# Optimization experiments

Measured on AMD Instinct MI355X. Metric: run time of the kernel, lower is better.

The kernel has to match this reference:

```python
import jax, jax.numpy as jnp
import numpy as np

N = 2048      # number of ROIs
C = 1024      # in_channels == inter_channels
G = 16        # groups
D = C // G    # per-group dim = 64


def _bbox_overlaps(b1, b2):
    # mmdet-1.x IoU with +1 pixel convention; b1:(N,4), b2:(M,4)
    area1 = (b1[:, 2] - b1[:, 0] + 1) * (b1[:, 3] - b1[:, 1] + 1)  # (N,)
    area2 = (b2[:, 2] - b2[:, 0] + 1) * (b2[:, 3] - b2[:, 1] + 1)  # (M,)
    lt = jnp.maximum(b1[:, None, :2], b2[None, :, :2])             # (N,M,2)
    rb = jnp.minimum(b1[:, None, 2:], b2[None, :, 2:])             # (N,M,2)
    wh = jnp.clip(rb - lt + 1, 0)
    inter = wh[..., 0] * wh[..., 1]                                # (N,M)
    return inter / (area1[:, None] + area2[None, :] - inter)


def setup_inputs() -> dict:
    key = jax.random.key(0)
    ks = jax.random.split(key, 9)
    in_x = jax.random.normal(ks[0], (N, C), dtype=jnp.float32)
    # valid boxes: [batch_idx, x1, y1, x2, y2]
    xy = jax.random.uniform(ks[1], (N, 2), minval=0.0, maxval=800.0)
    wh = jax.random.uniform(ks[2], (N, 2), minval=8.0, maxval=200.0)
    rois = jnp.concatenate([jnp.zeros((N, 1)), xy, xy + wh], axis=1).astype(jnp.float32)
    s = 1.0 / np.sqrt(C)
    W0 = jax.random.normal(ks[3], (C, C), dtype=jnp.float32) * s
    b0 = jnp.zeros((C,), dtype=jnp.float32)
    W1 = jax.random.normal(ks[4], (C, C), dtype=jnp.float32) * s
    b1 = jnp.zeros((C,), dtype=jnp.float32)
    # grouped 1x1 conv: per group maps C channels -> D channels
    Wout = jax.random.normal(ks[5], (G, D, C), dtype=jnp.float32) * s
    bout = jnp.zeros((C,), dtype=jnp.float32)
    return {"in_x": in_x, "rois": rois, "W0": W0, "b0": b0, "W1": W1,
            "b1": b1, "Wout": Wout, "bout": bout}


def reference(in_x, rois, W0, b0, W1, b1, Wout, bout):
    # self-attention path: in_ref_x = in_x, ref_rois = rois
    # embed convs are pre-activation (relu -> 1x1 conv), shared for x and ref_x
    def embed(v):
        v = jax.nn.relu(v) @ W0.T + b0
        v = jax.nn.relu(v) @ W1.T + b1
        return v
    x = embed(in_x)                      # (N, C)
    ref_x = x                            # shared convs, same input
    xg = x.reshape(N, G, D)
    rg = ref_x.reshape(N, G, D)
    scores = jnp.einsum('ngd,mgd->ngm', xg, rg) / jnp.sqrt(jnp.float32(D))  # (N,G,N)
    ious = _bbox_overlaps(rois[:, 1:], rois[:, 1:])                          # (N,N)
    scores = scores + jnp.log(ious[:, None, :] + 1e-6)
    attn = jax.nn.softmax(scores, axis=2)                                    # (N,G,N)
    y = jnp.einsum('ngm,mc->ngc', attn, in_x)                                # (N,G,C)
    out = jnp.einsum('ngc,goc->ngo', y, Wout).reshape(N, C) + bout           # (N,C)
    return out
```

## Files before the change

kernel.cpp:

```cpp
#include <hip/hip_runtime.h>
#include <math.h>

constexpr int NROI = 2048;
constexpr int CDIM = 1024;
constexpr int NG   = 16;
constexpr int DH   = 64;

typedef __attribute__((ext_vector_type(8))) short short8;
typedef __attribute__((ext_vector_type(4))) float floatx4;

#define MFMA_BF16(a, b, c) __builtin_amdgcn_mfma_f32_16x16x32_bf16((a), (b), (c), 0, 0, 0)

__device__ __forceinline__ short f2bf(float f) {
  unsigned u = __float_as_uint(f);
  unsigned r = 0x7fffu + ((u >> 16) & 1u);
  return (short)((u + r) >> 16);
}
__device__ __forceinline__ float bf2f(unsigned short u) {
  return __uint_as_float(((unsigned)u) << 16);
}
__device__ __forceinline__ unsigned pack2(float a, float b) {
  return (unsigned)(unsigned short)f2bf(a) | ((unsigned)(unsigned short)f2bf(b) << 16);
}

__device__ __forceinline__ unsigned cvtpk_bf16(float lo, float hi) {
  unsigned r;
  asm("v_cvt_pk_bf16_f32 %0, %1, %2" : "=v"(r) : "v"(lo), "v"(hi));
  return r;
}

__device__ __forceinline__ float fexp2(float x) {
#if __has_builtin(__builtin_amdgcn_exp2f)
  return __builtin_amdgcn_exp2f(x);
#else
  return __expf(x * 0.69314718056f);
#endif
}

typedef __attribute__((address_space(1))) void GV;
typedef __attribute__((address_space(3))) void LV;
__device__ __forceinline__ void gl2lds16(const void* g, void* l) {
  __builtin_amdgcn_global_load_lds((GV*)g, (LV*)l, 16, 0, 0);
}

__device__ __forceinline__ short8 brelu(short8 v) {
  union { short8 s; unsigned u[4]; } x; x.s = v;
#pragma unroll
  for (int i = 0; i < 4; ++i) {
    unsigned m = (x.u[i] >> 15) & 0x10001u;
    x.u[i] &= ~(m * 0xFFFFu);
  }
  return x.s;
}

__device__ __forceinline__ int keypos(int k) {
  return (k & ~31) | (((k >> 2) & 3) << 3) | (((k >> 4) & 1) << 2);
}

__global__ __launch_bounds__(256) void convert_kernel(
    const float* __restrict__ in_x, const float* __restrict__ W0,
    const float* __restrict__ W1, const float* __restrict__ Wout,
    short* __restrict__ xin_b, short* __restrict__ W0b,
    short* __restrict__ W1b, short* __restrict__ Woutb)
{
  const int i = blockIdx.x * 256 + threadIdx.x;
  {
    const float4 v = ((const float4*)in_x)[i];
    uint2 u; u.x = pack2(v.x, v.y); u.y = pack2(v.z, v.w);
    ((uint2*)xin_b)[i] = u;
  }
  if (i < 262144) {
    float4 v = ((const float4*)W0)[i];
    uint2 u; u.x = pack2(v.x, v.y); u.y = pack2(v.z, v.w);
    ((uint2*)W0b)[i] = u;
    v = ((const float4*)W1)[i];
    u.x = pack2(v.x, v.y); u.y = pack2(v.z, v.w);
    ((uint2*)W1b)[i] = u;
    v = ((const float4*)Wout)[i];
    u.x = pack2(v.x, v.y); u.y = pack2(v.z, v.w);
    ((uint2*)Woutb)[i] = u;
  }
}

__global__ __launch_bounds__(256) void iou4_kernel(const float* __restrict__ rois,
                                                   unsigned short* __restrict__ biasb)
{
  const int q  = blockIdx.y;
  const int k0 = (blockIdx.x * 256 + threadIdx.x) * 4;
  const float qx1 = rois[q * 5 + 1], qy1 = rois[q * 5 + 2];
  const float qx2 = rois[q * 5 + 3], qy2 = rois[q * 5 + 4];
  const float qa = (qx2 - qx1 + 1.f) * (qy2 - qy1 + 1.f);
  float v[4];
#pragma unroll
  for (int j = 0; j < 4; ++j) {
    const int k = k0 + j;
    const float kx1 = rois[k * 5 + 1], ky1 = rois[k * 5 + 2];
    const float kx2 = rois[k * 5 + 3], ky2 = rois[k * 5 + 4];
    const float ka = (kx2 - kx1 + 1.f) * (ky2 - ky1 + 1.f);
    float iw = fminf(qx2, kx2) - fmaxf(qx1, kx1) + 1.f;
    float ih = fminf(qy2, ky2) - fmaxf(qy1, ky1) + 1.f;
    iw = fmaxf(iw, 0.f); ih = fmaxf(ih, 0.f);
    const float inter = iw * ih;
    v[j] = inter * __builtin_amdgcn_rcpf(qa + ka - inter) + 1e-6f;
  }
  uint2 u; u.x = pack2(v[0], v[1]); u.y = pack2(v[2], v[3]);
  *(uint2*)&biasb[(size_t)q * NROI + keypos(k0)] = u;
}

template <int FUSED>
__global__ __launch_bounds__(256, 4) void gemm64(
    const short* __restrict__ A, const short* __restrict__ Ba,
    const short* __restrict__ Bb, const float* __restrict__ bias,
    short* __restrict__ outRM, short* __restrict__ outTR)
{
  __shared__ short As[2][8 * 512];
  __shared__ short Bs[2][8 * 512];
  const int t = threadIdx.x, w = t >> 6, lane = t & 63;
  const int wm = w >> 1, wn = w & 1;
  const int row0 = blockIdx.y * 64;
  bool isW0; int col0; const short* B;
  if (FUSED) {
    isW0 = blockIdx.x < 16;
    col0 = (blockIdx.x & 15) * 64;
    B = isW0 ? Ba : Bb;
  } else {
    isW0 = true; col0 = blockIdx.x * 64; B = Ba;
  }
  const bool doRelu = FUSED ? isW0 : true;
  const int rlo = lane & 15, khi = (lane >> 4) * 8;

  floatx4 acc[2][2];
#pragma unroll
  for (int i = 0; i < 2; ++i)
#pragma unroll
    for (int j = 0; j < 2; ++j) acc[i][j] = (floatx4){0.f, 0.f, 0.f, 0.f};

#pragma unroll
  for (int kh = 0; kh < 2; ++kh) {
    const int f = w * 2 + kh;
    gl2lds16(A + (size_t)(row0 + w * 16 + rlo) * CDIM + kh * 32 + khi, &As[0][f * 512]);
    gl2lds16(B + (size_t)(col0 + w * 16 + rlo) * CDIM + kh * 32 + khi, &Bs[0][f * 512]);
  }
  __syncthreads();

  for (int it = 0; it < 16; ++it) {
    const int p = it & 1;
    if (it < 15) {
      const int k1 = (it + 1) * 64;
#pragma unroll
      for (int kh = 0; kh < 2; ++kh) {
        const int f = w * 2 + kh;
        gl2lds16(A + (size_t)(row0 + w * 16 + rlo) * CDIM + k1 + kh * 32 + khi,
                 &As[1 - p][f * 512]);
        gl2lds16(B + (size_t)(col0 + w * 16 + rlo) * CDIM + k1 + kh * 32 + khi,
                 &Bs[1 - p][f * 512]);
      }
    }
#pragma unroll
    for (int kh = 0; kh < 2; ++kh) {
      short8 a[2], bf[2];
#pragma unroll
      for (int i = 0; i < 2; ++i) {
        a[i] = *(const short8*)&As[p][((wm * 2 + i) * 2 + kh) * 512 + lane * 8];
        if (doRelu) a[i] = brelu(a[i]);
      }
#pragma unroll
      for (int j = 0; j < 2; ++j)
        bf[j] = *(const short8*)&Bs[p][((wn * 2 + j) * 2 + kh) * 512 + lane * 8];
#pragma unroll
      for (int i = 0; i < 2; ++i)
#pragma unroll
        for (int j = 0; j < 2; ++j)
          acc[i][j] = MFMA_BF16(a[i], bf[j], acc[i][j]);
    }
    __syncthreads();
  }

  const int colL = lane & 15, qq = lane >> 4;
  if (!FUSED || isW0) {
    float bj[2];
    bj[0] = bias[col0 + wn * 32 + colL];
    bj[1] = bias[col0 + wn * 32 + 16 + colL];
#pragma unroll
    for (int i = 0; i < 2; ++i)
#pragma unroll
      for (int j = 0; j < 2; ++j)
#pragma unroll
        for (int r = 0; r < 4; ++r) {
          const int row = row0 + wm * 32 + i * 16 + qq * 4 + r;
          const int cc  = col0 + wn * 32 + j * 16 + colL;
          outRM[(size_t)row * CDIM + cc] = f2bf(acc[i][j][r] + bj[j]);
        }
  } else {
#pragma unroll
    for (int i = 0; i < 2; ++i)
#pragma unroll
      for (int j = 0; j < 2; ++j) {
        unsigned long long u =
            (unsigned long long)pack2(acc[i][j][0], acc[i][j][1]) |
            ((unsigned long long)pack2(acc[i][j][2], acc[i][j][3]) << 32);
        const int cc  = col0 + wn * 32 + j * 16 + colL;
        const int row = row0 + wm * 32 + i * 16 + qq * 4;
        *(unsigned long long*)&outTR[(size_t)cc * NROI + keypos(row)] = u;
      }
  }
}

__global__ __launch_bounds__(512, 4) void attn_bias(
    const short* __restrict__ Xb,
    const short* __restrict__ ZTb,
    const unsigned short* __restrict__ biasb,
    const float* __restrict__ bout,
    float* __restrict__ Out)
{
  const int lin  = blockIdx.x + 32 * blockIdx.y;
  const int xcd  = lin & 7;
  const int slot = lin >> 3;
  const int g    = 2 * xcd + (slot >> 5);
  const int n0   = (slot & 31) * 64;

  const int t    = threadIdx.x;
  const int w    = t >> 6;
  const int half = w >> 2;
  const int wq   = w & 3;
  const int lane = t & 63;
  const int col  = lane & 15;
  const int qq   = lane >> 4;
  const int rlo  = col, khi = qq * 8;

  __shared__ short Kf[2][2][4096];
  __shared__ short Vf[2][2][4096];

  const size_t qoff = (size_t)(n0 + wq * 16 + col) * CDIM + g * DH;
  const short8 qf0 = *(const short8*)(Xb + qoff + qq * 8);
  const short8 qf1 = *(const short8*)(Xb + qoff + 32 + qq * 8);

  floatx4 oc[4];
#pragma unroll
  for (int dt = 0; dt < 4; ++dt) oc[dt] = (floatx4){0.f, 0.f, 0.f, 0.f};
  float lsum = 0.f;

  const int mbase = half * 1024;
#pragma unroll
  for (int kh = 0; kh < 2; ++kh) {
    gl2lds16(Xb + (size_t)(mbase + wq * 16 + rlo) * CDIM + g * DH + kh * 32 + khi,
             &Kf[half][0][(wq * 2 + kh) * 512]);
    gl2lds16(ZTb + (size_t)(g * DH + wq * 16 + rlo) * NROI + mbase + kh * 32 + khi,
             &Vf[half][0][(wq * 2 + kh) * 512]);
  }
  __syncthreads();

  const unsigned short* bq =
      biasb + (size_t)(n0 + wq * 16 + col) * NROI + mbase + qq * 8;

  for (int it = 0; it < 16; ++it) {
    const int p  = it & 1;
    const int m0 = mbase + it * 64;

    union { short8 s[2]; unsigned short h[16]; } BU;
    BU.s[0] = *(const short8*)(bq + it * 64);
    BU.s[1] = *(const short8*)(bq + it * 64 + 32);

    if (it + 1 < 16) {
      const int m1 = m0 + 64;
#pragma unroll
      for (int kh = 0; kh < 2; ++kh) {
        gl2lds16(Xb + (size_t)(m1 + wq * 16 + rlo) * CDIM + g * DH + kh * 32 + khi,
                 &Kf[half][1 - p][(wq * 2 + kh) * 512]);
        gl2lds16(ZTb + (size_t)(g * DH + wq * 16 + rlo) * NROI + m1 + kh * 32 + khi,
                 &Vf[half][1 - p][(wq * 2 + kh) * 512]);
      }
    }

    float e[4][4];
    __builtin_amdgcn_s_setprio(1);
#pragma unroll
    for (int ct = 0; ct < 4; ++ct) {
      const short8 k0 = *(const short8*)&Kf[half][p][(ct * 2 + 0) * 512 + lane * 8];
      const short8 k1 = *(const short8*)&Kf[half][p][(ct * 2 + 1) * 512 + lane * 8];
      floatx4 z4 = (floatx4){0.f, 0.f, 0.f, 0.f};
      z4 = MFMA_BF16(k0, qf0, z4);
      z4 = MFMA_BF16(k1, qf1, z4);
#pragma unroll
      for (int r = 0; r < 4; ++r) e[ct][r] = z4[r];
    }
    __builtin_amdgcn_s_setprio(0);

#pragma unroll
    for (int ct = 0; ct < 4; ++ct)
#pragma unroll
      for (int r = 0; r < 4; ++r) {
        const float pv = fexp2(e[ct][r] * 0.18033688011f) * bf2f(BU.h[ct * 4 + r]);
        e[ct][r] = pv;
        lsum += pv;
      }

    union { short8 s; unsigned u[4]; } U0, U1;
#pragma unroll
    for (int j = 0; j < 2; ++j) {
      U0.u[j * 2 + 0] = cvtpk_bf16(e[j][0], e[j][1]);
      U0.u[j * 2 + 1] = cvtpk_bf16(e[j][2], e[j][3]);
      U1.u[j * 2 + 0] = cvtpk_bf16(e[j + 2][0], e[j + 2][1]);
      U1.u[j * 2 + 1] = cvtpk_bf16(e[j + 2][2], e[j + 2][3]);
    }

    __builtin_amdgcn_s_setprio(1);
#pragma unroll
    for (int dt = 0; dt < 4; ++dt) {
      const short8 v0 = *(const short8*)&Vf[half][p][(dt * 2 + 0) * 512 + lane * 8];
      const short8 v1 = *(const short8*)&Vf[half][p][(dt * 2 + 1) * 512 + lane * 8];
      oc[dt] = MFMA_BF16(U0.s, v0, oc[dt]);
      oc[dt] = MFMA_BF16(U1.s, v1, oc[dt]);
    }
    __builtin_amdgcn_s_setprio(0);
    __syncthreads();
  }

  float s = lsum;
  s += __shfl_xor(s, 16);
  s += __shfl_xor(s, 32);

  float* ocb = (float*)&Kf[0][0][0];
  float* lsb = (float*)&Vf[0][0][0];
  const int cbase = (wq * 64 + lane) * 16;
  if (half) {
#pragma unroll
    for (int dt = 0; dt < 4; ++dt)
#pragma unroll
      for (int r = 0; r < 4; ++r) ocb[cbase + dt * 4 + r] = oc[dt][r];
    lsb[wq * 64 + lane] = s;
  }
  __syncthreads();
  if (!half) {
    s += lsb[wq * 64 + lane];
    float ls[4], rinv[4];
#pragma unroll
    for (int r = 0; r < 4; ++r)
      ls[r] = __shfl(s, (qq << 4) | (qq * 4 + r));
#pragma unroll
    for (int r = 0; r < 4; ++r)
      rinv[r] = __builtin_amdgcn_rcpf(ls[r]);
#pragma unroll
    for (int dt = 0; dt < 4; ++dt) {
      const float bo = bout[g * DH + dt * 16 + col];
#pragma unroll
      for (int r = 0; r < 4; ++r)
        Out[(size_t)(n0 + wq * 16 + qq * 4 + r) * CDIM + g * DH + dt * 16 + col] =
            (oc[dt][r] + ocb[cbase + dt * 4 + r]) * rinv[r] + bo;
    }
  }
}

extern "C" void kernel_launch(void* const* d_in, const int* in_sizes, int n_in,
                              void* d_out, int out_size, void* d_ws, size_t ws_size,
                              hipStream_t stream) {
  const float* in_x = (const float*)d_in[0];
  const float* rois = (const float*)d_in[1];
  const float* W0   = (const float*)d_in[2];
  const float* b0   = (const float*)d_in[3];
  const float* W1   = (const float*)d_in[4];
  const float* b1   = (const float*)d_in[5];
  const float* Wout = (const float*)d_in[6];
  const float* bout = (const float*)d_in[7];
  char* w8 = (char*)d_ws;

  short* xin_b = (short*)w8;
  short* W0b   = (short*)(w8 + ((size_t)4 << 20));
  short* W1b   = (short*)(w8 + ((size_t)6 << 20));
  short* Woutb = (short*)(w8 + ((size_t)8 << 20));
  short* zT    = (short*)(w8 + ((size_t)10 << 20));
  unsigned short* biasb = (unsigned short*)(w8 + ((size_t)14 << 20));
  short* xb  = xin_b;
  short* t0b = (short*)d_out;

  convert_kernel<<<2048, 256, 0, stream>>>(in_x, W0, W1, Wout,
                                           xin_b, W0b, W1b, Woutb);
  iou4_kernel<<<dim3(2, NROI), 256, 0, stream>>>(rois, biasb);
  gemm64<1><<<dim3(32, 32), 256, 0, stream>>>(xin_b, W0b, Woutb, b0, t0b, zT);
  gemm64<0><<<dim3(16, 32), 256, 0, stream>>>(t0b, W1b, nullptr, b1, xb, nullptr);
  attn_bias<<<dim3(32, NG), 512, 0, stream>>>(xb, zT, biasb, bout,
                                              (float*)d_out);
}
```

Baseline: 191.0 us.

## Widen attention block to 128 queries with 4-way key split

Each attention block now handles 128 query rows over 1024 threads. Every wave computes two 16-row query sub-tiles against each staged K/V tile, and the key range is split into four 512-key quarters instead of two halves. This doubles reuse of each LDS K/V tile per MFMA and halves the grid to 256 blocks. It also fuses the exp/bias step into the QK loop and drops the setprio hints. In exchange it needs more registers and a larger 4-way cross-wave reduction through LDS, and 256 large blocks may underfill the GPU.

```diff
diff --git a/kernel.cpp b/kernel.cpp
--- a/kernel.cpp
+++ b/kernel.cpp
@@ -206,147 +206,170 @@
   }
 }
 
-__global__ __launch_bounds__(512, 4) void attn_bias(
+__global__ __launch_bounds__(1024) void attn_bias(
     const short* __restrict__ Xb,
     const short* __restrict__ ZTb,
     const unsigned short* __restrict__ biasb,
     const float* __restrict__ bout,
     float* __restrict__ Out)
 {
-  const int lin  = blockIdx.x + 32 * blockIdx.y;
+  const int lin  = blockIdx.x + 16 * blockIdx.y;
   const int xcd  = lin & 7;
   const int slot = lin >> 3;
-  const int g    = 2 * xcd + (slot >> 5);
-  const int n0   = (slot & 31) * 64;
+  const int g    = 2 * xcd + (slot >> 4);
+  const int n0   = (slot & 15) * 128;
 
   const int t    = threadIdx.x;
   const int w    = t >> 6;
-  const int half = w >> 2;
+  const int qt   = w >> 2;
   const int wq   = w & 3;
   const int lane = t & 63;
   const int col  = lane & 15;
   const int qq   = lane >> 4;
   const int rlo  = col, khi = qq * 8;
 
-  __shared__ short Kf[2][2][4096];
-  __shared__ short Vf[2][2][4096];
-
-  const size_t qoff = (size_t)(n0 + wq * 16 + col) * CDIM + g * DH;
-  const short8 qf0 = *(const short8*)(Xb + qoff + qq * 8);
-  const short8 qf1 = *(const short8*)(Xb + qoff + 32 + qq * 8);
-
-  floatx4 oc[4];
-#pragma unroll
-  for (int dt = 0; dt < 4; ++dt) oc[dt] = (floatx4){0.f, 0.f, 0.f, 0.f};
-  float lsum = 0.f;
-
-  const int mbase = half * 1024;
+  __shared__ short Kq[4][2][4096];
+  __shared__ short Vq[4][2][4096];
+
+  short8 qf[2][2];
+#pragma unroll
+  for (int s = 0; s < 2; ++s) {
+    const size_t qoff = (size_t)(n0 + wq * 32 + s * 16 + col) * CDIM + g * DH;
+    qf[s][0] = *(const short8*)(Xb + qoff + qq * 8);
+    qf[s][1] = *(const short8*)(Xb + qoff + 32 + qq * 8);
+  }
+
+  floatx4 oc[2][4];
+#pragma unroll
+  for (int s = 0; s < 2; ++s)
+#pragma unroll
+    for (int dt = 0; dt < 4; ++dt) oc[s][dt] = (floatx4){0.f, 0.f, 0.f, 0.f};
+  float lsum[2] = {0.f, 0.f};
+
+  const int kb = qt * 512;
+
 #pragma unroll
   for (int kh = 0; kh < 2; ++kh) {
-    gl2lds16(Xb + (size_t)(mbase + wq * 16 + rlo) * CDIM + g * DH + kh * 32 + khi,
-             &Kf[half][0][(wq * 2 + kh) * 512]);
-    gl2lds16(ZTb + (size_t)(g * DH + wq * 16 + rlo) * NROI + mbase + kh * 32 + khi,
-             &Vf[half][0][(wq * 2 + kh) * 512]);
+    gl2lds16(Xb + (size_t)(kb + wq * 16 + rlo) * CDIM + g * DH + kh * 32 + khi,
+             &Kq[qt][0][(wq * 2 + kh) * 512]);
+    gl2lds16(ZTb + (size_t)(g * DH + wq * 16 + rlo) * NROI + kb + kh * 32 + khi,
+             &Vq[qt][0][(wq * 2 + kh) * 512]);
   }
   __syncthreads();
 
-  const unsigned short* bq =
-      biasb + (size_t)(n0 + wq * 16 + col) * NROI + mbase + qq * 8;
-
-  for (int it = 0; it < 16; ++it) {
+  const unsigned short* bq0 =
+      biasb + (size_t)(n0 + wq * 32 + col) * NROI + kb + qq * 8;
+  const unsigned short* bq1 = bq0 + (size_t)16 * NROI;
+
+  for (int it = 0; it < 8; ++it) {
     const int p  = it & 1;
-    const int m0 = mbase + it * 64;
-
-    union { short8 s[2]; unsigned short h[16]; } BU;
-    BU.s[0] = *(const short8*)(bq + it * 64);
-    BU.s[1] = *(const short8*)(bq + it * 64 + 32);
-
-    if (it + 1 < 16) {
+    const int m0 = kb + it * 64;
+
+    union { short8 s8[4]; unsigned short h[32]; } BU;
+    BU.s8[0] = *(const short8*)(bq0 + it * 64);
+    BU.s8[1] = *(const short8*)(bq0 + it * 64 + 32);
+    BU.s8[2] = *(const short8*)(bq1 + it * 64);
+    BU.s8[3] = *(const short8*)(bq1 + it * 64 + 32);
+
+    if (it + 1 < 8) {
       const int m1 = m0 + 64;
 #pragma unroll
       for (int kh = 0; kh < 2; ++kh) {
         gl2lds16(Xb + (size_t)(m1 + wq * 16 + rlo) * CDIM + g * DH + kh * 32 + khi,
-                 &Kf[half][1 - p][(wq * 2 + kh) * 512]);
+                 &Kq[qt][1 - p][(wq * 2 + kh) * 512]);
         gl2lds16(ZTb + (size_t)(g * DH + wq * 16 + rlo) * NROI + m1 + kh * 32 + khi,
-                 &Vf[half][1 - p][(wq * 2 + kh) * 512]);
-      }
-    }
-
-    float e[4][4];
-    __builtin_amdgcn_s_setprio(1);
+                 &Vq[qt][1 - p][(wq * 2 + kh) * 512]);
+      }
+    }
+
+    union { short8 s; unsigned u[4]; } U[2][2];
 #pragma unroll
     for (int ct = 0; ct < 4; ++ct) {
-      const short8 k0 = *(const short8*)&Kf[half][p][(ct * 2 + 0) * 512 + lane * 8];
-      const short8 k1 = *(const short8*)&Kf[half][p][(ct * 2 + 1) * 512 + lane * 8];
-      floatx4 z4 = (floatx4){0.f, 0.f, 0.f, 0.f};
-      z4 = MFMA_BF16(k0, qf0, z4);
-      z4 = MFMA_BF16(k1, qf1, z4);
-#pragma unroll
-      for (int r = 0; r < 4; ++r) e[ct][r] = z4[r];
-    }
-    __builtin_amdgcn_s_setprio(0);
-
-#pragma unroll
-    for (int ct = 0; ct < 4; ++ct)
+      const short8 k0 = *(const short8*)&Kq[qt][p][(ct * 2 + 0) * 512 + lane * 8];
+      const short8 k1 = *(const short8*)&Kq[qt][p][(ct * 2 + 1) * 512 + lane * 8];
+#pragma unroll
+      for (int s = 0; s < 2; ++s) {
+        floatx4 z4 = (floatx4){0.f, 0.f, 0.f, 0.f};
+        z4 = MFMA_BF16(k0, qf[s][0], z4);
+        z4 = MFMA_BF16(k1, qf[s][1], z4);
+        float pv0 = fexp2(z4[0] * 0.18033688011f) * bf2f(BU.h[s * 16 + ct * 4 + 0]);
+        float pv1 = fexp2(z4[1] * 0.18033688011f) * bf2f(BU.h[s * 16 + ct * 4 + 1]);
+        float pv2 = fexp2(z4[2] * 0.18033688011f) * bf2f(BU.h[s * 16 + ct * 4 + 2]);
+        float pv3 = fexp2(z4[3] * 0.18033688011f) * bf2f(BU.h[s * 16 + ct * 4 + 3]);
+        lsum[s] += (pv0 + pv1) + (pv2 + pv3);
+        U[s][ct >> 1].u[(ct & 1) * 2 + 0] = cvtpk_bf16(pv0, pv1);
+        U[s][ct >> 1].u[(ct & 1) * 2 + 1] = cvtpk_bf16(pv2, pv3);
+      }
+    }
+
+#pragma unroll
+    for (int dt = 0; dt < 4; ++dt) {
+      const short8 v0 = *(const short8*)&Vq[qt][p][(dt * 2 + 0) * 512 + lane * 8];
+      const short8 v1 = *(const short8*)&Vq[qt][p][(dt * 2 + 1) * 512 + lane * 8];
+#pragma unroll
+      for (int s = 0; s < 2; ++s) {
+        oc[s][dt] = MFMA_BF16(U[s][0].s, v0, oc[s][dt]);
+        oc[s][dt] = MFMA_BF16(U[s][1].s, v1, oc[s][dt]);
+      }
+    }
+    __syncthreads();
+  }
+
+  float ssum[2];
+#pragma unroll
+  for (int s = 0; s < 2; ++s) {
+    float x = lsum[s];
+    x += __shfl_xor(x, 16);
+    x += __shfl_xor(x, 32);
+    ssum[s] = x;
+  }
+
+  float* kbuf = (float*)&Kq[0][0][0];
+  float* vbuf = (float*)&Vq[0][0][0];
+  const int wslot = (qt - 1) * 4 + wq;
+  if (qt != 0) {
+#pragma unroll
+    for (int dt = 0; dt < 4; ++dt)
 #pragma unroll
       for (int r = 0; r < 4; ++r) {
-        const float pv = fexp2(e[ct][r] * 0.18033688011f) * bf2f(BU.h[ct * 4 + r]);
-        e[ct][r] = pv;
-        lsum += pv;
-      }
-
-    union { short8 s; unsigned u[4]; } U0, U1;
-#pragma unroll
-    for (int j = 0; j < 2; ++j) {
-      U0.u[j * 2 + 0] = cvtpk_bf16(e[j][0], e[j][1]);
-      U0.u[j * 2 + 1] = cvtpk_bf16(e[j][2], e[j][3]);
-      U1.u[j * 2 + 0] = cvtpk_bf16(e[j + 2][0], e[j + 2][1]);
-      U1.u[j * 2 + 1] = cvtpk_bf16(e[j + 2][2], e[j + 2][3]);
-    }
-
-    __builtin_amdgcn_s_setprio(1);
-#pragma unroll
-    for (int dt = 0; dt < 4; ++dt) {
-      const short8 v0 = *(const short8*)&Vf[half][p][(dt * 2 + 0) * 512 + lane * 8];
-      const short8 v1 = *(const short8*)&Vf[half][p][(dt * 2 + 1) * 512 + lane * 8];
-      oc[dt] = MFMA_BF16(U0.s, v0, oc[dt]);
-      oc[dt] = MFMA_BF16(U1.s, v1, oc[dt]);
-    }
-    __builtin_amdgcn_s_setprio(0);
-    __syncthreads();
-  }
-
-  float s = lsum;
-  s += __shfl_xor(s, 16);
-  s += __shfl_xor(s, 32);
-
-  float* ocb = (float*)&Kf[0][0][0];
-  float* lsb = (float*)&Vf[0][0][0];
-  const int cbase = (wq * 64 + lane) * 16;
-  if (half) {
-#pragma unroll
-    for (int dt = 0; dt < 4; ++dt)
-#pragma unroll
-      for (int r = 0; r < 4; ++r) ocb[cbase + dt * 4 + r] = oc[dt][r];
-    lsb[wq * 64 + lane] = s;
+        kbuf[(dt * 4 + r) * 768 + wslot * 64 + lane] = oc[0][dt][r];
+        vbuf[(dt * 4 + r) * 768 + wslot * 64 + lane] = oc[1][dt][r];
+      }
+    kbuf[12288 + (0 * 12 + wslot) * 64 + lane] = ssum[0];
+    kbuf[12288 + (1 * 12 + wslot) * 64 + lane] = ssum[1];
   }
   __syncthreads();
-  if (!half) {
-    s += lsb[wq * 64 + lane];
-    float ls[4], rinv[4];
-#pragma unroll
-    for (int r = 0; r < 4; ++r)
-      ls[r] = __shfl(s, (qq << 4) | (qq * 4 + r));
-#pragma unroll
-    for (int r = 0; r < 4; ++r)
-      rinv[r] = __builtin_amdgcn_rcpf(ls[r]);
-#pragma unroll
-    for (int dt = 0; dt < 4; ++dt) {
-      const float bo = bout[g * DH + dt * 16 + col];
+  if (qt == 0) {
+#pragma unroll
+    for (int j = 0; j < 3; ++j) {
+      const int ws = j * 4 + wq;
+#pragma unroll
+      for (int dt = 0; dt < 4; ++dt)
+#pragma unroll
+        for (int r = 0; r < 4; ++r) {
+          oc[0][dt][r] += kbuf[(dt * 4 + r) * 768 + ws * 64 + lane];
+          oc[1][dt][r] += vbuf[(dt * 4 + r) * 768 + ws * 64 + lane];
+        }
+      ssum[0] += kbuf[12288 + (0 * 12 + ws) * 64 + lane];
+      ssum[1] += kbuf[12288 + (1 * 12 + ws) * 64 + lane];
+    }
+#pragma unroll
+    for (int s = 0; s < 2; ++s) {
+      float ls[4], rinv[4];
 #pragma unroll
       for (int r = 0; r < 4; ++r)
-        Out[(size_t)(n0 + wq * 16 + qq * 4 + r) * CDIM + g * DH + dt * 16 + col] =
-            (oc[dt][r] + ocb[cbase + dt * 4 + r]) * rinv[r] + bo;
+        ls[r] = __shfl(ssum[s], (qq << 4) | (qq * 4 + r));
+#pragma unroll
+      for (int r = 0; r < 4; ++r)
+        rinv[r] = __builtin_amdgcn_rcpf(ls[r]);
+#pragma unroll
+      for (int dt = 0; dt < 4; ++dt) {
+        const float bo = bout[g * DH + dt * 16 + col];
+#pragma unroll
+        for (int r = 0; r < 4; ++r)
+          Out[(size_t)(n0 + wq * 32 + s * 16 + qq * 4 + r) * CDIM + g * DH +
+              dt * 16 + col] = oc[s][dt][r] * rinv[r] + bo;
+      }
     }
   }
 }
@@ -378,6 +401,6 @@
   iou4_kernel<<<dim3(2, NROI), 256, 0, stream>>>(rois, biasb);
   gemm64<1><<<dim3(32, 32), 256, 0, stream>>>(xin_b, W0b, Woutb, b0, t0b, zT);
   gemm64<0><<<dim3(16, 32), 256, 0, stream>>>(t0b, W1b, nullptr, b1, xb, nullptr);
-  attn_bias<<<dim3(32, NG), 512, 0, stream>>>(xb, zT, biasb, bout,
-                                              (float*)d_out);
-}
+  attn_bias<<<dim3(16, 16), 1024, 0, stream>>>(xb, zT, biasb, bout,
+                                               (float*)d_out);
+}
```

Result: faster. 180.2 us (-5.7%).
